# Performance work log

Measured on AMD Instinct MI355X. Metric: run time of the kernel, lower is better.

The kernel has to match this reference:

```python
import jax, jax.numpy as jnp
import numpy as np

N = 100000   # nodes
E = 1000000  # edges
D = 128      # hidden dim (all n_hidden entries)
ED = 21      # edge_dim hard-coded in the module


def setup_inputs() -> dict:
    key = jax.random.key(0)
    ks = jax.random.split(key, 32)
    w = lambda k, shape: (jax.random.normal(k, shape, dtype=jnp.float32) * 0.05)
    inp = {
        "G": jax.random.normal(ks[0], (N, D), dtype=jnp.float32),
        "edge_index": jax.random.randint(ks[1], (2, E), 0, N),
        "edge_attribute": jax.random.normal(ks[2], (E, ED), dtype=jnp.float32),
        # 3-layer node embedding MLP (stacked since all dims are D)
        "emb_W": w(ks[3], (3, D, D)), "emb_b": w(ks[4], (3, D)),
        # 2 ResGatedGraphConv layers (conv3 is unused in forward)
        "key_W": w(ks[5], (2, D, D)), "key_b": w(ks[6], (2, D)),
        "qry_W": w(ks[7], (2, D, D)), "qry_b": w(ks[8], (2, D)),
        "val_W": w(ks[9], (2, D, D)), "val_b": w(ks[10], (2, D)),
        "skp_W": w(ks[11], (2, D, D)), "skp_b": w(ks[12], (2, D)),
        "edg_W": w(ks[13], (2, ED, D)), "edg_b": w(ks[14], (2, D)),
        # graph linears
        "g1_W": w(ks[15], (D, D)), "g1_b": w(ks[16], (D,)),
        "g2_W": w(ks[17], (D, D)), "g2_b": w(ks[18], (D,)),
        # head: concat(node, graph_mean) -> 2D -> D -> D -> 1
        "h1_W": w(ks[19], (2 * D, D)), "h1_b": w(ks[20], (D,)),
        "h2_W": w(ks[21], (D, D)), "h2_b": w(ks[22], (D,)),
        "h3_W": w(ks[23], (D, 1)), "h3_b": w(ks[24], (1,)),
    }
    return inp


def reference(G, edge_index, edge_attribute,
              emb_W, emb_b, key_W, key_b, qry_W, qry_b, val_W, val_b,
              skp_W, skp_b, edg_W, edg_b,
              g1_W, g1_b, g2_W, g2_b, h1_W, h1_b, h2_W, h2_b, h3_W, h3_b):
    x = G
    # embedding MLP: Linear -> ReLU x3
    for i in range(3):
        x = jax.nn.relu(x @ emb_W[i] + emb_b[i])
    src, dst = edge_index[0], edge_index[1]
    # ResGatedGraphConv (PyG): out_i = W_skip x_i + sum_j sigmoid(k_i + q_j + W_e e_ij) * v_j
    for i in range(2):
        k = x @ key_W[i] + key_b[i]   # per target node i
        q = x @ qry_W[i] + qry_b[i]   # per source node j
        v = x @ val_W[i] + val_b[i]
        eta = jax.nn.sigmoid(k[dst] + q[src] + edge_attribute @ edg_W[i] + edg_b[i])  # [E, D]
        agg = jax.ops.segment_sum(eta * v[src], dst, num_segments=N)  # scatter-add [N, D]
        x = jax.nn.relu(agg + x @ skp_W[i] + skp_b[i])
    x = jax.nn.relu(x @ g1_W + g1_b)
    x = x @ g2_W + g2_b
    # per-node concat with mean-pooled graph embedding (vectorized form of the Python loop)
    gmean = jnp.mean(x, axis=0)
    u = jnp.concatenate([x, jnp.broadcast_to(gmean, x.shape)], axis=-1)  # [N, 2D]
    u = jax.nn.relu(u @ h1_W + h1_b)
    u = jax.nn.relu(u @ h2_W + h2_b)
    return u @ h3_W + h3_b  # [N, 1]
```

## Files before the change

kernel.cpp:

```cpp
#include <hip/hip_runtime.h>
#include <hip/hip_bf16.h>

#define DD 128
#define LW 136

typedef __attribute__((ext_vector_type(8))) short bf16x8;
typedef __attribute__((ext_vector_type(4))) float f32x4;

__device__ __forceinline__ void cvt8(const float4 a0, const float4 a1,
                                     bf16x8& hi, bf16x8& lo)
{
    float af[8] = {a0.x, a0.y, a0.z, a0.w, a1.x, a1.y, a1.z, a1.w};
    union { unsigned int u[4]; bf16x8 v; } H, L;
    #pragma unroll
    for (int i = 0; i < 4; ++i) {
        unsigned int b0 = __float_as_uint(af[2*i]);
        unsigned int b1 = __float_as_uint(af[2*i+1]);
        unsigned int h0 = b0 & 0xFFFF0000u;
        unsigned int h1 = b1 & 0xFFFF0000u;
        H.u[i] = (h0 >> 16) | h1;
        float r0 = af[2*i]   - __uint_as_float(h0);
        float r1 = af[2*i+1] - __uint_as_float(h1);
        L.u[i] = (__float_as_uint(r0) >> 16) | (__float_as_uint(r1) & 0xFFFF0000u);
    }
    hi = H.v; lo = L.v;
}

__global__ __launch_bounds__(256) void gemm_mfma(
    const float* __restrict__ X, const unsigned short* __restrict__ Wt,
    const float* __restrict__ bias, float* __restrict__ Y,
    int N, int ldY, int act)
{
    const int lane = threadIdx.x & 63;
    const int wid  = threadIdx.x >> 6;
    const int wr = wid >> 1, wc = wid & 1;
    const int row0 = blockIdx.x * 128 + wr * 64;
    const int cb   = blockIdx.y;
    const unsigned short* WtH = Wt + (size_t)cb * 32768;
    const unsigned short* WtL = WtH + 16384;

    const int l15 = lane & 15;
    const int kg  = (lane >> 4) * 8;

    f32x4 acc[4][4] = {};

    int arow[4];
    #pragma unroll
    for (int mi = 0; mi < 4; ++mi) {
        int r = row0 + mi * 16 + l15;
        arow[mi] = r < N ? r : N - 1;
    }

    #pragma unroll
    for (int kc = 0; kc < 4; ++kc) {
        const int kb = kc * 32 + kg;
        bf16x8 ah[4], al[4], bh[4], bl[4];
        #pragma unroll
        for (int mi = 0; mi < 4; ++mi) {
            const float* p = X + (size_t)arow[mi] * DD + kb;
            float4 a0 = *(const float4*)p;
            float4 a1 = *(const float4*)(p + 4);
            cvt8(a0, a1, ah[mi], al[mi]);
        }
        #pragma unroll
        for (int ni = 0; ni < 4; ++ni) {
            int m = wc * 64 + ni * 16 + l15;
            bh[ni] = *(const bf16x8*)(WtH + (size_t)m * DD + kb);
            bl[ni] = *(const bf16x8*)(WtL + (size_t)m * DD + kb);
        }
        #pragma unroll
        for (int mi = 0; mi < 4; ++mi)
            #pragma unroll
            for (int ni = 0; ni < 4; ++ni) {
                acc[mi][ni] = __builtin_amdgcn_mfma_f32_16x16x32_bf16(ah[mi], bh[ni], acc[mi][ni], 0, 0, 0);
                acc[mi][ni] = __builtin_amdgcn_mfma_f32_16x16x32_bf16(ah[mi], bl[ni], acc[mi][ni], 0, 0, 0);
                acc[mi][ni] = __builtin_amdgcn_mfma_f32_16x16x32_bf16(al[mi], bh[ni], acc[mi][ni], 0, 0, 0);
            }
    }

    const int colW = cb * 128 + wc * 64;
    #pragma unroll
    for (int ni = 0; ni < 4; ++ni) {
        float bv = bias[colW + ni * 16 + l15];
        #pragma unroll
        for (int mi = 0; mi < 4; ++mi) {
            #pragma unroll
            for (int r = 0; r < 4; ++r) {
                int row = row0 + mi * 16 + (lane >> 4) * 4 + r;
                if (row < N) {
                    float v = acc[mi][ni][r] + bv;
                    Y[(size_t)row * ldY + colW + ni * 16 + l15] = act ? fmaxf(v, 0.f) : v;
                }
            }
        }
    }
}

__device__ __forceinline__ void mfma_step(
    const unsigned short* __restrict__ WH, const unsigned short* __restrict__ WL,
    int wavecol, int l15, int kb,
    const bf16x8 ah[4], const bf16x8 al[4], f32x4 acc[4][2])
{
    bf16x8 bh[2], bl[2];
    #pragma unroll
    for (int ni = 0; ni < 2; ++ni) {
        int m = wavecol + ni * 16 + l15;
        bh[ni] = *(const bf16x8*)(WH + (size_t)m * DD + kb);
        bl[ni] = *(const bf16x8*)(WL + (size_t)m * DD + kb);
    }
    #pragma unroll
    for (int mi = 0; mi < 4; ++mi)
        #pragma unroll
        for (int ni = 0; ni < 2; ++ni) {
            acc[mi][ni] = __builtin_amdgcn_mfma_f32_16x16x32_bf16(ah[mi], bh[ni], acc[mi][ni], 0, 0, 0);
            acc[mi][ni] = __builtin_amdgcn_mfma_f32_16x16x32_bf16(ah[mi], bl[ni], acc[mi][ni], 0, 0, 0);
            acc[mi][ni] = __builtin_amdgcn_mfma_f32_16x16x32_bf16(al[mi], bh[ni], acc[mi][ni], 0, 0, 0);
        }
}

__device__ __forceinline__ void glb_layer(
    const float* __restrict__ X, const int arow[4],
    const unsigned short* __restrict__ WU,
    int wavecol, int l15, int kg, f32x4 acc[4][2])
{
    const unsigned short* WH = WU;
    const unsigned short* WL = WU + 16384;
    #pragma unroll
    for (int kc = 0; kc < 4; ++kc) {
        const int kb = kc * 32 + kg;
        bf16x8 ah[4], al[4];
        #pragma unroll
        for (int mi = 0; mi < 4; ++mi) {
            const float* p = X + (size_t)arow[mi] * DD + kb;
            float4 a0 = *(const float4*)p;
            float4 a1 = *(const float4*)(p + 4);
            cvt8(a0, a1, ah[mi], al[mi]);
        }
        mfma_step(WH, WL, wavecol, l15, kb, ah, al, acc);
    }
}

__device__ __forceinline__ void lds_layer(
    const unsigned short (*AH)[LW], const unsigned short (*AL)[LW],
    const unsigned short* __restrict__ WU,
    int wavecol, int l15, int kg, f32x4 acc[4][2])
{
    const unsigned short* WH = WU;
    const unsigned short* WL = WU + 16384;
    #pragma unroll
    for (int kc = 0; kc < 4; ++kc) {
        const int kb = kc * 32 + kg;
        bf16x8 ah[4], al[4];
        #pragma unroll
        for (int mi = 0; mi < 4; ++mi) {
            ah[mi] = *(const bf16x8*)&AH[mi * 16 + l15][kb];
            al[mi] = *(const bf16x8*)&AL[mi * 16 + l15][kb];
        }
        mfma_step(WH, WL, wavecol, l15, kb, ah, al, acc);
    }
}

__device__ __forceinline__ void epi_lds(
    const f32x4 acc[4][2], unsigned short (*AH)[LW], unsigned short (*AL)[LW],
    const float* __restrict__ bias, int wavecol, int l15, int rg, int relu)
{
    #pragma unroll
    for (int ni = 0; ni < 2; ++ni) {
        const int col = wavecol + ni * 16 + l15;
        const float bv = bias[col];
        #pragma unroll
        for (int mi = 0; mi < 4; ++mi)
            #pragma unroll
            for (int r = 0; r < 4; ++r) {
                const int row = mi * 16 + rg + r;
                float v = acc[mi][ni][r] + bv;
                if (relu) v = fmaxf(v, 0.f);
                unsigned int u = __float_as_uint(v), h = u & 0xFFFF0000u;
                float res = v - __uint_as_float(h);
                AH[row][col] = (unsigned short)(h >> 16);
                AL[row][col] = (unsigned short)(__float_as_uint(res) >> 16);
            }
    }
}

__global__ __launch_bounds__(256) void fused_emb3(
    const float* __restrict__ G, const unsigned short* __restrict__ Wt,
    const float* __restrict__ embb, float* __restrict__ Y, int N)
{
    __shared__ unsigned short AH[64][LW], AL[64][LW];
    const int lane = threadIdx.x & 63, wid = threadIdx.x >> 6;
    const int wavecol = wid * 32;
    const int l15 = lane & 15, kg = (lane >> 4) * 8, rg = (lane >> 4) * 4;
    const int row0 = blockIdx.x * 64;

    int arow[4];
    #pragma unroll
    for (int mi = 0; mi < 4; ++mi) {
        int r = row0 + mi * 16 + l15;
        arow[mi] = r < N ? r : N - 1;
    }

    f32x4 acc[4][2] = {};
    glb_layer(G, arow, Wt, wavecol, l15, kg, acc);
    epi_lds(acc, AH, AL, embb, wavecol, l15, rg, 1);
    __syncthreads();

    #pragma unroll
    for (int mi = 0; mi < 4; ++mi)
        #pragma unroll
        for (int ni = 0; ni < 2; ++ni) acc[mi][ni] = (f32x4){0,0,0,0};
    lds_layer(AH, AL, Wt + 32768, wavecol, l15, kg, acc);
    __syncthreads();
    epi_lds(acc, AH, AL, embb + 128, wavecol, l15, rg, 1);
    __syncthreads();

    #pragma unroll
    for (int mi = 0; mi < 4; ++mi)
        #pragma unroll
        for (int ni = 0; ni < 2; ++ni) acc[mi][ni] = (f32x4){0,0,0,0};
    lds_layer(AH, AL, Wt + 65536, wavecol, l15, kg, acc);

    #pragma unroll
    for (int ni = 0; ni < 2; ++ni) {
        const int col = wavecol + ni * 16 + l15;
        const float bv = embb[256 + col];
        #pragma unroll
        for (int mi = 0; mi < 4; ++mi)
            #pragma unroll
            for (int r = 0; r < 4; ++r) {
                int row = row0 + mi * 16 + rg + r;
                if (row < N)
                    Y[(size_t)row * DD + col] = fmaxf(acc[mi][ni][r] + bv, 0.f);
            }
    }
}

__global__ __launch_bounds__(256) void fused_g12(
    const float* __restrict__ X, const unsigned short* __restrict__ Wt,
    const float* __restrict__ g1b, const float* __restrict__ g2b,
    float* __restrict__ Y, float* __restrict__ gsum, int N)
{
    __shared__ unsigned short AH[64][LW], AL[64][LW];
    __shared__ float csum[128];
    const int tid = threadIdx.x;
    const int lane = tid & 63, wid = tid >> 6;
    const int wavecol = wid * 32;
    const int l15 = lane & 15, kg = (lane >> 4) * 8, rg = (lane >> 4) * 4;
    const int row0 = blockIdx.x * 64;

    if (tid < 128) csum[tid] = 0.f;

    int arow[4];
    #pragma unroll
    for (int mi = 0; mi < 4; ++mi) {
        int r = row0 + mi * 16 + l15;
        arow[mi] = r < N ? r : N - 1;
    }

    f32x4 acc[4][2] = {};
    glb_layer(X, arow, Wt, wavecol, l15, kg, acc);
    epi_lds(acc, AH, AL, g1b, wavecol, l15, rg, 1);
    __syncthreads();

    #pragma unroll
    for (int mi = 0; mi < 4; ++mi)
        #pragma unroll
        for (int ni = 0; ni < 2; ++ni) acc[mi][ni] = (f32x4){0,0,0,0};
    lds_layer(AH, AL, Wt + 32768, wavecol, l15, kg, acc);

    #pragma unroll
    for (int ni = 0; ni < 2; ++ni) {
        const int col = wavecol + ni * 16 + l15;
        const float bv = g2b[col];
        float part = 0.f;
        #pragma unroll
        for (int mi = 0; mi < 4; ++mi)
            #pragma unroll
            for (int r = 0; r < 4; ++r) {
                int row = row0 + mi * 16 + rg + r;
                if (row < N) {
                    float v = acc[mi][ni][r] + bv;
                    Y[(size_t)row * DD + col] = v;
                    part += v;
                }
            }
        atomicAdd(&csum[col], part);
    }
    __syncthreads();
    if (tid < 128) atomicAdd(&gsum[tid], csum[tid]);
}

__global__ __launch_bounds__(256) void fused_head(
    const float* __restrict__ X, const unsigned short* __restrict__ Wt,
    const float* __restrict__ cvec, const float* __restrict__ h2b,
    const float* __restrict__ h3w, const float* __restrict__ h3b,
    float* __restrict__ out, int N)
{
    __shared__ unsigned short AH[64][LW], AL[64][LW];
    const int tid = threadIdx.x;
    const int lane = tid & 63, wid = tid >> 6;
    const int wavecol = wid * 32;
    const int l15 = lane & 15, kg = (lane >> 4) * 8, rg = (lane >> 4) * 4;
    const int row0 = blockIdx.x * 64;

    int arow[4];
    #pragma unroll
    for (int mi = 0; mi < 4; ++mi) {
        int r = row0 + mi * 16 + l15;
        arow[mi] = r < N ? r : N - 1;
    }

    f32x4 acc[4][2] = {};
    glb_layer(X, arow, Wt, wavecol, l15, kg, acc);
    epi_lds(acc, AH, AL, cvec, wavecol, l15, rg, 1);
    __syncthreads();

    #pragma unroll
    for (int mi = 0; mi < 4; ++mi)
        #pragma unroll
        for (int ni = 0; ni < 2; ++ni) acc[mi][ni] = (f32x4){0,0,0,0};
    lds_layer(AH, AL, Wt + 32768, wavecol, l15, kg, acc);
    __syncthreads();
    epi_lds(acc, AH, AL, h2b, wavecol, l15, rg, 1);
    __syncthreads();

    const int row = tid >> 2, seg = tid & 3;
    float s = 0.f;
    #pragma unroll 8
    for (int j = 0; j < 32; ++j) {
        int col = seg * 32 + j;
        float xv = __uint_as_float((unsigned int)AH[row][col] << 16)
                 + __uint_as_float((unsigned int)AL[row][col] << 16);
        s = fmaf(xv, h3w[col], s);
    }
    s += __shfl_xor(s, 1, 64);
    s += __shfl_xor(s, 2, 64);
    if (seg == 0 && row0 + row < N) out[row0 + row] = s + h3b[0];
}

__global__ __launch_bounds__(256) void prep_weights(
    const float* __restrict__ embW, const float* __restrict__ keyW,
    const float* __restrict__ qryW, const float* __restrict__ valW,
    const float* __restrict__ skpW, const float* __restrict__ g1W,
    const float* __restrict__ g2W, const float* __restrict__ h1W,
    const float* __restrict__ h2W,
    const float* __restrict__ keyb, const float* __restrict__ qryb,
    const float* __restrict__ valb, const float* __restrict__ skpb,
    unsigned short* __restrict__ Wt, float* __restrict__ biasCat)
{
    const int u = blockIdx.x;
    const int t = threadIdx.x;
    __shared__ float T[128][129];

    const float* src;
    if (u < 3)       src = embW + (size_t)u * 16384;
    else if (u < 7)  { const float* p[4] = {keyW, qryW, valW, skpW}; src = p[u - 3]; }
    else if (u < 11) { const float* p[4] = {keyW, qryW, valW, skpW}; src = p[u - 7] + 16384; }
    else if (u == 11) src = g1W;
    else if (u == 12) src = g2W;
    else if (u == 13) src = h1W;
    else              src = h2W;

    #pragma unroll
    for (int i = 0; i < 64; ++i) {
        int idx = t + 256 * i;
        T[idx >> 7][idx & 127] = src[idx];
    }
    __syncthreads();

    unsigned short* dH = Wt + (size_t)u * 32768;
    unsigned short* dL = dH + 16384;
    const int m = t >> 1, kbase = (t & 1) * 64;
    for (int j = 0; j < 64; ++j) {
        int k = kbase + j;
        float a = T[k][m];
        unsigned int b = __float_as_uint(a);
        unsigned int h = b & 0xFFFF0000u;
        float r = a - __uint_as_float(h);
        dH[m * 128 + k] = (unsigned short)(h >> 16);
        dL[m * 128 + k] = (unsigned short)(__float_as_uint(r) >> 16);
    }

    if (u == 0) {
        for (int x = t; x < 1024; x += 256) {
            int L = x >> 9, c = x & 511;
            const float* bp = (c < 128) ? keyb : (c < 256) ? qryb : (c < 384) ? valb : skpb;
            biasCat[x] = bp[L * 128 + (c & 127)];
        }
    }
}

__global__ void hist_kernel(const int* __restrict__ dstA, int* __restrict__ hist, int E)
{
    for (int e = blockIdx.x * blockDim.x + threadIdx.x; e < E;
         e += gridDim.x * blockDim.x)
        atomicAdd(&hist[dstA[e]], 1);
}

__global__ __launch_bounds__(256) void scan1_kernel(
    const int* __restrict__ in, int n_in,
    int* __restrict__ out, int* __restrict__ bsum, int n)
{
    __shared__ int wtot[4];
    const int t = threadIdx.x, lane = t & 63, wv = t >> 6;
    const int base = blockIdx.x * 1024 + t * 4;
    int v[4]; int sum = 0;
    #pragma unroll
    for (int j = 0; j < 4; ++j) {
        int idx = base + j;
        v[j] = (idx < n_in) ? in[idx] : 0;
        sum += v[j];
    }
    int incl = sum;
    #pragma unroll
    for (int d = 1; d < 64; d <<= 1) {
        int y = __shfl_up(incl, d, 64);
        if (lane >= d) incl += y;
    }
    if (lane == 63) wtot[wv] = incl;
    __syncthreads();
    int woff = 0;
    for (int w = 0; w < wv; ++w) woff += wtot[w];
    int run = woff + incl - sum;
    #pragma unroll
    for (int j = 0; j < 4; ++j) {
        int idx = base + j;
        if (idx < n) out[idx] = run;
        run += v[j];
    }
    if (t == 0)
        bsum[blockIdx.x] = wtot[0] + wtot[1] + wtot[2] + wtot[3];
}

__global__ void scan2_kernel(int* __restrict__ bsum, int nb)
{
    if (blockIdx.x == 0 && threadIdx.x == 0) {
        int run = 0;
        for (int i = 0; i < nb; ++i) { int t = bsum[i]; bsum[i] = run; run += t; }
    }
}

__global__ __launch_bounds__(256) void scan3_kernel(
    int* __restrict__ out, const int* __restrict__ bsum,
    int* __restrict__ cursor, int n, int n_nodes)
{
    const int base = blockIdx.x * 1024 + threadIdx.x * 4;
    const int add = bsum[blockIdx.x];
    #pragma unroll
    for (int j = 0; j < 4; ++j) {
        int idx = base + j;
        if (idx < n) {
            int vv = out[idx] + add;
            out[idx] = vv;
            if (idx < n_nodes) cursor[idx] = vv;
        }
    }
}

__global__ void scatter_kernel(const int* __restrict__ srcA, const int* __restrict__ dstA,
                               int* __restrict__ cursor, int* __restrict__ perm,
                               int* __restrict__ srcp, int E)
{
    for (int e = blockIdx.x * blockDim.x + threadIdx.x; e < E;
         e += gridDim.x * blockDim.x) {
        int d = dstA[e];
        int pos = atomicAdd(&cursor[d], 1);
        perm[pos] = e;
        srcp[pos] = srcA[e];
    }
}

__global__ __launch_bounds__(256) void edge_agg9(
    const int* __restrict__ row_ptr, const int* __restrict__ srcp,
    const float* __restrict__ ea, const int* __restrict__ perm,
    const float* __restrict__ We, const float* __restrict__ be,
    const float* __restrict__ fused, float* __restrict__ X, int N)
{
    const int wv = threadIdx.x >> 6, lane = threadIdx.x & 63;
    const int d = blockIdx.x * 4 + wv;
    if (d >= N) return;
    const int c = lane * 2;

    float2 w[21];
    #pragma unroll
    for (int j = 0; j < 21; ++j)
        w[j] = *(const float2*)(We + j * DD + c);
    const float2 b2 = *(const float2*)(be + c);
    const float2 kd = *(const float2*)(fused + (size_t)d * 512 + c);
    const float2 sk = *(const float2*)(fused + (size_t)d * 512 + 384 + c);

    float ax = 0.f, ay = 0.f;
    const int i0 = __builtin_amdgcn_readfirstlane(row_ptr[d]);
    const int i1 = __builtin_amdgcn_readfirstlane(row_ptr[d + 1]);

    for (int i = i0; i < i1; i += 2) {
        const int iA = i;
        const int iB = (i + 1 < i1) ? i + 1 : i1 - 1;
        const float wgtB = (i + 1 < i1) ? 1.f : 0.f;

        const int sA = __builtin_amdgcn_readfirstlane(srcp[iA]);
        const int sB = __builtin_amdgcn_readfirstlane(srcp[iB]);
        const int pA = __builtin_amdgcn_readfirstlane(perm[iA]);
        const int pB = __builtin_amdgcn_readfirstlane(perm[iB]);

        const float* eA = ea + (size_t)pA * 21;
        const float* eB = ea + (size_t)pB * 21;
        float aA[21], aB[21];
        #pragma unroll
        for (int j = 0; j < 21; ++j) { aA[j] = eA[j]; aB[j] = eB[j]; }

        const float* fpA = fused + (size_t)sA * 512;
        const float* fpB = fused + (size_t)sB * 512;
        float2 qA = *(const float2*)(fpA + 128 + c);
        float2 vA = *(const float2*)(fpA + 256 + c);
        float2 qB = *(const float2*)(fpB + 128 + c);
        float2 vB = *(const float2*)(fpB + 256 + c);

        float pxA[4] = {0,0,0,0}, pyA[4] = {0,0,0,0};
        float pxB[4] = {0,0,0,0}, pyB[4] = {0,0,0,0};
        #pragma unroll
        for (int j = 0; j < 21; ++j) {
            int s = j & 3;
            pxA[s] = fmaf(aA[j], w[j].x, pxA[s]);
            pyA[s] = fmaf(aA[j], w[j].y, pyA[s]);
            pxB[s] = fmaf(aB[j], w[j].x, pxB[s]);
            pyB[s] = fmaf(aB[j], w[j].y, pyB[s]);
        }
        float exA = (pxA[0] + pxA[1]) + (pxA[2] + pxA[3]) + b2.x;
        float eyA = (pyA[0] + pyA[1]) + (pyA[2] + pyA[3]) + b2.y;
        float exB = (pxB[0] + pxB[1]) + (pxB[2] + pxB[3]) + b2.x;
        float eyB = (pyB[0] + pyB[1]) + (pyB[2] + pyB[3]) + b2.y;

        float zxA = kd.x + qA.x + exA;
        float zyA = kd.y + qA.y + eyA;
        float zxB = kd.x + qB.x + exB;
        float zyB = kd.y + qB.y + eyB;

        float gxA = 1.f / (1.f + __expf(-zxA));
        float gyA = 1.f / (1.f + __expf(-zyA));
        float gxB = wgtB / (1.f + __expf(-zxB));
        float gyB = wgtB / (1.f + __expf(-zyB));

        ax = fmaf(gxA, vA.x, ax);
        ay = fmaf(gyA, vA.y, ay);
        ax = fmaf(gxB, vB.x, ax);
        ay = fmaf(gyB, vB.y, ay);
    }

    X[(size_t)d * DD + c]     = fmaxf(ax + sk.x, 0.f);
    X[(size_t)d * DD + c + 1] = fmaxf(ay + sk.y, 0.f);
}

__global__ void cvec_kernel(const float* __restrict__ gsum, const float* __restrict__ h1W,
                            const float* __restrict__ h1b, float* __restrict__ cvec, float invN)
{
    const int m = threadIdx.x;
    float acc = h1b[m];
    for (int k = 0; k < 128; ++k)
        acc = fmaf(gsum[k] * invN, h1W[(size_t)(128 + k) * DD + m], acc);
    cvec[m] = acc;
}

extern "C" void kernel_launch(void* const* d_in, const int* in_sizes, int n_in,
                              void* d_out, int out_size, void* d_ws, size_t ws_size,
                              hipStream_t stream)
{
    const float* G    = (const float*)d_in[0];
    const int*   ei   = (const int*)  d_in[1];
    const float* ea   = (const float*)d_in[2];
    const float* embW = (const float*)d_in[3];
    const float* embb = (const float*)d_in[4];
    const float* keyW = (const float*)d_in[5];
    const float* keyb = (const float*)d_in[6];
    const float* qryW = (const float*)d_in[7];
    const float* qryb = (const float*)d_in[8];
    const float* valW = (const float*)d_in[9];
    const float* valb = (const float*)d_in[10];
    const float* skpW = (const float*)d_in[11];
    const float* skpb = (const float*)d_in[12];
    const float* edgW = (const float*)d_in[13];
    const float* edgb = (const float*)d_in[14];
    const float* g1W  = (const float*)d_in[15];
    const float* g1b  = (const float*)d_in[16];
    const float* g2W  = (const float*)d_in[17];
    const float* g2b  = (const float*)d_in[18];
    const float* h1W  = (const float*)d_in[19];
    const float* h1b  = (const float*)d_in[20];
    const float* h2W  = (const float*)d_in[21];
    const float* h2b  = (const float*)d_in[22];
    const float* h3W  = (const float*)d_in[23];
    const float* h3b  = (const float*)d_in[24];

    const int N = in_sizes[0] / DD;
    const int E = in_sizes[2] / 21;
    const int* srcA = ei;
    const int* dstA = ei + E;

    const size_t S = (size_t)N * DD;
    float* bx     = (float*)d_ws;
    float* b2     = bx + S;
    float* bfused = b2 + S;
    float* gsum   = bfused + (size_t)N * 512;
    float* cvec   = gsum + DD;
    float* biasCat= cvec + DD;
    unsigned short* Wt = (unsigned short*)(biasCat + 1024);
    int* hist = (int*)((char*)Wt + (size_t)15 * 32768 * 2);
    int* row  = hist + N;
    int* cur  = row + N + 1;
    int* bsum = cur + N;
    int* perm = bsum + 128;
    int* srcp = perm + E;

    const dim3 g4grid((N + 127) / 128, 4);
    const int fgrid   = (N + 63) / 64;
    const int aggGrid = (N + 3) / 4;
    const int nScan = N + 1;
    const int nb = (nScan + 1023) / 1024;

    prep_weights<<<15, 256, 0, stream>>>(embW, keyW, qryW, valW, skpW,
                                         g1W, g2W, h1W, h2W,
                                         keyb, qryb, valb, skpb, Wt, biasCat);
    hipMemsetAsync(hist, 0, (size_t)N * sizeof(int), stream);
    hipMemsetAsync(gsum, 0, DD * sizeof(float), stream);
    hist_kernel<<<1024, 256, 0, stream>>>(dstA, hist, E);
    scan1_kernel<<<nb, 256, 0, stream>>>(hist, N, row, bsum, nScan);
    scan2_kernel<<<1, 64, 0, stream>>>(bsum, nb);
    scan3_kernel<<<nb, 256, 0, stream>>>(row, bsum, cur, nScan, N);
    scatter_kernel<<<1024, 256, 0, stream>>>(srcA, dstA, cur, perm, srcp, E);

    #define UNIT(u) (Wt + (size_t)(u) * 32768)

    fused_emb3<<<fgrid, 256, 0, stream>>>(G, UNIT(0), embb, bx, N);

    gemm_mfma<<<g4grid, 256, 0, stream>>>(bx, UNIT(3), biasCat, bfused, N, 512, 0);
    edge_agg9<<<aggGrid, 256, 0, stream>>>(row, srcp, ea, perm,
                                           edgW + 0, edgb + 0, bfused, b2, N);

    gemm_mfma<<<g4grid, 256, 0, stream>>>(b2, UNIT(7), biasCat + 512, bfused, N, 512, 0);
    edge_agg9<<<aggGrid, 256, 0, stream>>>(row, srcp, ea, perm,
                                           edgW + 21*DD, edgb + DD, bfused, bx, N);

    fused_g12<<<fgrid, 256, 0, stream>>>(bx, UNIT(11), g1b, g2b, b2, gsum, N);

    cvec_kernel<<<1, DD, 0, stream>>>(gsum, h1W, h1b, cvec, 1.0f / (float)N);

    fused_head<<<fgrid, 256, 0, stream>>>(b2, UNIT(13), cvec, h2b, h3W, h3b,
                                          (float*)d_out, N);
}
```

Before: 1.229 ms.

## Split each destination node across two wavefronts, one column per lane

The edge aggregation kernel now assigns two wavefronts per destination node, each handling 64 columns with one float per lane, instead of one wavefront with float2 per lane. This doubles the number of wavefronts so more gathers are in flight, and halves per-lane FMA and sigmoid work and register use. In exchange, the per-edge scalar loads (src, perm, the 21 edge attributes) and the row-pointer reads are duplicated across the two wavefronts, and the gather loads become narrower.

```diff
diff --git a/kernel.cpp b/kernel.cpp
--- a/kernel.cpp
+++ b/kernel.cpp
@@ -470,26 +470,26 @@
     }
 }
 
-__global__ __launch_bounds__(256) void edge_agg9(
+__global__ __launch_bounds__(256) void edge_agg10(
     const int* __restrict__ row_ptr, const int* __restrict__ srcp,
     const float* __restrict__ ea, const int* __restrict__ perm,
     const float* __restrict__ We, const float* __restrict__ be,
     const float* __restrict__ fused, float* __restrict__ X, int N)
 {
     const int wv = threadIdx.x >> 6, lane = threadIdx.x & 63;
-    const int d = blockIdx.x * 4 + wv;
+    const int d = blockIdx.x * 2 + (wv >> 1);
     if (d >= N) return;
-    const int c = lane * 2;
-
-    float2 w[21];
+    const int col = (wv & 1) * 64 + lane;
+
+    float w[21];
     #pragma unroll
     for (int j = 0; j < 21; ++j)
-        w[j] = *(const float2*)(We + j * DD + c);
-    const float2 b2 = *(const float2*)(be + c);
-    const float2 kd = *(const float2*)(fused + (size_t)d * 512 + c);
-    const float2 sk = *(const float2*)(fused + (size_t)d * 512 + 384 + c);
-
-    float ax = 0.f, ay = 0.f;
+        w[j] = We[j * DD + col];
+    const float bb = be[col];
+    const float kd = fused[(size_t)d * 512 + col];
+    const float sk = fused[(size_t)d * 512 + 384 + col];
+
+    float ax = 0.f;
     const int i0 = __builtin_amdgcn_readfirstlane(row_ptr[d]);
     const int i1 = __builtin_amdgcn_readfirstlane(row_ptr[d + 1]);
 
@@ -511,44 +511,32 @@
 
         const float* fpA = fused + (size_t)sA * 512;
         const float* fpB = fused + (size_t)sB * 512;
-        float2 qA = *(const float2*)(fpA + 128 + c);
-        float2 vA = *(const float2*)(fpA + 256 + c);
-        float2 qB = *(const float2*)(fpB + 128 + c);
-        float2 vB = *(const float2*)(fpB + 256 + c);
-
-        float pxA[4] = {0,0,0,0}, pyA[4] = {0,0,0,0};
-        float pxB[4] = {0,0,0,0}, pyB[4] = {0,0,0,0};
+        float qA = fpA[128 + col];
+        float vA = fpA[256 + col];
+        float qB = fpB[128 + col];
+        float vB = fpB[256 + col];
+
+        float pxA[4] = {0,0,0,0}, pxB[4] = {0,0,0,0};
         #pragma unroll
         for (int j = 0; j < 21; ++j) {
             int s = j & 3;
-            pxA[s] = fmaf(aA[j], w[j].x, pxA[s]);
-            pyA[s] = fmaf(aA[j], w[j].y, pyA[s]);
-            pxB[s] = fmaf(aB[j], w[j].x, pxB[s]);
-            pyB[s] = fmaf(aB[j], w[j].y, pyB[s]);
-        }
-        float exA = (pxA[0] + pxA[1]) + (pxA[2] + pxA[3]) + b2.x;
-        float eyA = (pyA[0] + pyA[1]) + (pyA[2] + pyA[3]) + b2.y;
-        float exB = (pxB[0] + pxB[1]) + (pxB[2] + pxB[3]) + b2.x;
-        float eyB = (pyB[0] + pyB[1]) + (pyB[2] + pyB[3]) + b2.y;
-
-        float zxA = kd.x + qA.x + exA;
-        float zyA = kd.y + qA.y + eyA;
-        float zxB = kd.x + qB.x + exB;
-        float zyB = kd.y + qB.y + eyB;
+            pxA[s] = fmaf(aA[j], w[j], pxA[s]);
+            pxB[s] = fmaf(aB[j], w[j], pxB[s]);
+        }
+        float exA = (pxA[0] + pxA[1]) + (pxA[2] + pxA[3]) + bb;
+        float exB = (pxB[0] + pxB[1]) + (pxB[2] + pxB[3]) + bb;
+
+        float zxA = kd + qA + exA;
+        float zxB = kd + qB + exB;
 
         float gxA = 1.f / (1.f + __expf(-zxA));
-        float gyA = 1.f / (1.f + __expf(-zyA));
         float gxB = wgtB / (1.f + __expf(-zxB));
-        float gyB = wgtB / (1.f + __expf(-zyB));
-
-        ax = fmaf(gxA, vA.x, ax);
-        ay = fmaf(gyA, vA.y, ay);
-        ax = fmaf(gxB, vB.x, ax);
-        ay = fmaf(gyB, vB.y, ay);
-    }
-
-    X[(size_t)d * DD + c]     = fmaxf(ax + sk.x, 0.f);
-    X[(size_t)d * DD + c + 1] = fmaxf(ay + sk.y, 0.f);
+
+        ax = fmaf(gxA, vA, ax);
+        ax = fmaf(gxB, vB, ax);
+    }
+
+    X[(size_t)d * DD + col] = fmaxf(ax + sk, 0.f);
 }
 
 __global__ void cvec_kernel(const float* __restrict__ gsum, const float* __restrict__ h1W,
@@ -613,7 +601,7 @@
 
     const dim3 g4grid((N + 127) / 128, 4);
     const int fgrid   = (N + 63) / 64;
-    const int aggGrid = (N + 3) / 4;
+    const int aggGrid = (N + 1) / 2;
     const int nScan = N + 1;
     const int nb = (nScan + 1023) / 1024;
 
@@ -633,12 +621,12 @@
     fused_emb3<<<fgrid, 256, 0, stream>>>(G, UNIT(0), embb, bx, N);
 
     gemm_mfma<<<g4grid, 256, 0, stream>>>(bx, UNIT(3), biasCat, bfused, N, 512, 0);
-    edge_agg9<<<aggGrid, 256, 0, stream>>>(row, srcp, ea, perm,
-                                           edgW + 0, edgb + 0, bfused, b2, N);
+    edge_agg10<<<aggGrid, 256, 0, stream>>>(row, srcp, ea, perm,
+                                            edgW + 0, edgb + 0, bfused, b2, N);
 
     gemm_mfma<<<g4grid, 256, 0, stream>>>(b2, UNIT(7), biasCat + 512, bfused, N, 512, 0);
-    edge_agg9<<<aggGrid, 256, 0, stream>>>(row, srcp, ea, perm,
-                                           edgW + 21*DD, edgb + DD, bfused, bx, N);
+    edge_agg10<<<aggGrid, 256, 0, stream>>>(row, srcp, ea, perm,
+                                            edgW + 21*DD, edgb + DD, bfused, bx, N);
 
     fused_g12<<<fgrid, 256, 0, stream>>>(bx, UNIT(11), g1b, g2b, b2, gsum, N);
 
```

Measured after the change: 1.253 ms. About the same (+1.9%).

## Fuse key/query/value/skip projection into embedding MLP kernel and LDS-staged GEMM

Applied to the files above, without the earlier changes.

The first conv layer's four projections (key, query, value, skip) are now computed inside the embedding-MLP kernel from the LDS-resident activations, so the intermediate node embedding is never written to or reread from global memory. The second layer's projection GEMM is replaced by a kernel that converts a 64-row tile to split bf16 in LDS once and reuses it for all four 128-column weight blocks. This drops a full N×128 write/read round trip and the repeated per-column-block conversion of X. In exchange each block does four times more serial MFMA work with smaller tiles and a serial loop over column blocks, which may lower parallelism per launch.

```diff
diff --git a/kernel.cpp b/kernel.cpp
--- a/kernel.cpp
+++ b/kernel.cpp
@@ -24,76 +24,6 @@
         L.u[i] = (__float_as_uint(r0) >> 16) | (__float_as_uint(r1) & 0xFFFF0000u);
     }
     hi = H.v; lo = L.v;
-}
-
-__global__ __launch_bounds__(256) void gemm_mfma(
-    const float* __restrict__ X, const unsigned short* __restrict__ Wt,
-    const float* __restrict__ bias, float* __restrict__ Y,
-    int N, int ldY, int act)
-{
-    const int lane = threadIdx.x & 63;
-    const int wid  = threadIdx.x >> 6;
-    const int wr = wid >> 1, wc = wid & 1;
-    const int row0 = blockIdx.x * 128 + wr * 64;
-    const int cb   = blockIdx.y;
-    const unsigned short* WtH = Wt + (size_t)cb * 32768;
-    const unsigned short* WtL = WtH + 16384;
-
-    const int l15 = lane & 15;
-    const int kg  = (lane >> 4) * 8;
-
-    f32x4 acc[4][4] = {};
-
-    int arow[4];
-    #pragma unroll
-    for (int mi = 0; mi < 4; ++mi) {
-        int r = row0 + mi * 16 + l15;
-        arow[mi] = r < N ? r : N - 1;
-    }
-
-    #pragma unroll
-    for (int kc = 0; kc < 4; ++kc) {
-        const int kb = kc * 32 + kg;
-        bf16x8 ah[4], al[4], bh[4], bl[4];
-        #pragma unroll
-        for (int mi = 0; mi < 4; ++mi) {
-            const float* p = X + (size_t)arow[mi] * DD + kb;
-            float4 a0 = *(const float4*)p;
-            float4 a1 = *(const float4*)(p + 4);
-            cvt8(a0, a1, ah[mi], al[mi]);
-        }
-        #pragma unroll
-        for (int ni = 0; ni < 4; ++ni) {
-            int m = wc * 64 + ni * 16 + l15;
-            bh[ni] = *(const bf16x8*)(WtH + (size_t)m * DD + kb);
-            bl[ni] = *(const bf16x8*)(WtL + (size_t)m * DD + kb);
-        }
-        #pragma unroll
-        for (int mi = 0; mi < 4; ++mi)
-            #pragma unroll
-            for (int ni = 0; ni < 4; ++ni) {
-                acc[mi][ni] = __builtin_amdgcn_mfma_f32_16x16x32_bf16(ah[mi], bh[ni], acc[mi][ni], 0, 0, 0);
-                acc[mi][ni] = __builtin_amdgcn_mfma_f32_16x16x32_bf16(ah[mi], bl[ni], acc[mi][ni], 0, 0, 0);
-                acc[mi][ni] = __builtin_amdgcn_mfma_f32_16x16x32_bf16(al[mi], bh[ni], acc[mi][ni], 0, 0, 0);
-            }
-    }
-
-    const int colW = cb * 128 + wc * 64;
-    #pragma unroll
-    for (int ni = 0; ni < 4; ++ni) {
-        float bv = bias[colW + ni * 16 + l15];
-        #pragma unroll
-        for (int mi = 0; mi < 4; ++mi) {
-            #pragma unroll
-            for (int r = 0; r < 4; ++r) {
-                int row = row0 + mi * 16 + (lane >> 4) * 4 + r;
-                if (row < N) {
-                    float v = acc[mi][ni][r] + bv;
-                    Y[(size_t)row * ldY + colW + ni * 16 + l15] = act ? fmaxf(v, 0.f) : v;
-                }
-            }
-        }
-    }
 }
 
 __device__ __forceinline__ void mfma_step(
@@ -183,9 +113,10 @@
     }
 }
 
-__global__ __launch_bounds__(256) void fused_emb3(
+__global__ __launch_bounds__(256) void fused_emb3q(
     const float* __restrict__ G, const unsigned short* __restrict__ Wt,
-    const float* __restrict__ embb, float* __restrict__ Y, int N)
+    const float* __restrict__ embb, const float* __restrict__ biasCat,
+    float* __restrict__ bfused, int N)
 {
     __shared__ unsigned short AH[64][LW], AL[64][LW];
     const int lane = threadIdx.x & 63, wid = threadIdx.x >> 6;
@@ -219,19 +150,74 @@
         #pragma unroll
         for (int ni = 0; ni < 2; ++ni) acc[mi][ni] = (f32x4){0,0,0,0};
     lds_layer(AH, AL, Wt + 65536, wavecol, l15, kg, acc);
-
-    #pragma unroll
-    for (int ni = 0; ni < 2; ++ni) {
-        const int col = wavecol + ni * 16 + l15;
-        const float bv = embb[256 + col];
+    __syncthreads();
+    epi_lds(acc, AH, AL, embb + 256, wavecol, l15, rg, 1);
+    __syncthreads();
+
+    for (int cb = 0; cb < 4; ++cb) {
         #pragma unroll
         for (int mi = 0; mi < 4; ++mi)
             #pragma unroll
-            for (int r = 0; r < 4; ++r) {
-                int row = row0 + mi * 16 + rg + r;
-                if (row < N)
-                    Y[(size_t)row * DD + col] = fmaxf(acc[mi][ni][r] + bv, 0.f);
-            }
+            for (int ni = 0; ni < 2; ++ni) acc[mi][ni] = (f32x4){0,0,0,0};
+        lds_layer(AH, AL, Wt + (size_t)(3 + cb) * 32768, wavecol, l15, kg, acc);
+        #pragma unroll
+        for (int ni = 0; ni < 2; ++ni) {
+            const int gcol = cb * 128 + wavecol + ni * 16 + l15;
+            const float bv = biasCat[gcol];
+            #pragma unroll
+            for (int mi = 0; mi < 4; ++mi)
+                #pragma unroll
+                for (int r = 0; r < 4; ++r) {
+                    int row = row0 + mi * 16 + rg + r;
+                    if (row < N)
+                        bfused[(size_t)row * 512 + gcol] = acc[mi][ni][r] + bv;
+                }
+        }
+    }
+}
+
+__global__ __launch_bounds__(256) void fused_kqvs(
+    const float* __restrict__ X, const unsigned short* __restrict__ Wt,
+    const float* __restrict__ biasCat, float* __restrict__ bfused, int N)
+{
+    __shared__ unsigned short AH[64][LW], AL[64][LW];
+    const int tid = threadIdx.x;
+    const int lane = tid & 63, wid = tid >> 6;
+    const int wavecol = wid * 32;
+    const int l15 = lane & 15, kg = (lane >> 4) * 8, rg = (lane >> 4) * 4;
+    const int row0 = blockIdx.x * 64;
+
+    for (int idx = tid; idx < 64 * 128; idx += 256) {
+        const int row = idx >> 7, col = idx & 127;
+        int gr = row0 + row; if (gr >= N) gr = N - 1;
+        float v = X[(size_t)gr * DD + col];
+        unsigned int u = __float_as_uint(v), h = u & 0xFFFF0000u;
+        float res = v - __uint_as_float(h);
+        AH[row][col] = (unsigned short)(h >> 16);
+        AL[row][col] = (unsigned short)(__float_as_uint(res) >> 16);
+    }
+    __syncthreads();
+
+    f32x4 acc[4][2];
+    for (int cb = 0; cb < 4; ++cb) {
+        #pragma unroll
+        for (int mi = 0; mi < 4; ++mi)
+            #pragma unroll
+            for (int ni = 0; ni < 2; ++ni) acc[mi][ni] = (f32x4){0,0,0,0};
+        lds_layer(AH, AL, Wt + (size_t)cb * 32768, wavecol, l15, kg, acc);
+        #pragma unroll
+        for (int ni = 0; ni < 2; ++ni) {
+            const int gcol = cb * 128 + wavecol + ni * 16 + l15;
+            const float bv = biasCat[gcol];
+            #pragma unroll
+            for (int mi = 0; mi < 4; ++mi)
+                #pragma unroll
+                for (int r = 0; r < 4; ++r) {
+                    int row = row0 + mi * 16 + rg + r;
+                    if (row < N)
+                        bfused[(size_t)row * 512 + gcol] = acc[mi][ni][r] + bv;
+                }
+        }
     }
 }
 
@@ -611,7 +597,6 @@
     int* perm = bsum + 128;
     int* srcp = perm + E;
 
-    const dim3 g4grid((N + 127) / 128, 4);
     const int fgrid   = (N + 63) / 64;
     const int aggGrid = (N + 3) / 4;
     const int nScan = N + 1;
@@ -630,13 +615,12 @@
 
     #define UNIT(u) (Wt + (size_t)(u) * 32768)
 
-    fused_emb3<<<fgrid, 256, 0, stream>>>(G, UNIT(0), embb, bx, N);
-
-    gemm_mfma<<<g4grid, 256, 0, stream>>>(bx, UNIT(3), biasCat, bfused, N, 512, 0);
+    fused_emb3q<<<fgrid, 256, 0, stream>>>(G, Wt, embb, biasCat, bfused, N);
+
     edge_agg9<<<aggGrid, 256, 0, stream>>>(row, srcp, ea, perm,
                                            edgW + 0, edgb + 0, bfused, b2, N);
 
-    gemm_mfma<<<g4grid, 256, 0, stream>>>(b2, UNIT(7), biasCat + 512, bfused, N, 512, 0);
+    fused_kqvs<<<fgrid, 256, 0, stream>>>(b2, UNIT(7), biasCat + 512, bfused, N);
     edge_agg9<<<aggGrid, 256, 0, stream>>>(row, srcp, ea, perm,
                                            edgW + 21*DD, edgb + DD, bfused, bx, N);
 
```

Result: faster. 1.121 ms (-8.8%).
